# Performance work log

Measured on AMD Instinct MI355X. Metric: run time of the kernel, lower is better.

## Reference

```python
import jax, jax.numpy as jnp
import numpy as np
import math

D_IMG = 768
D_TXT = 512
EPS = 1e-5  # torch LayerNorm default


def setup_inputs() -> dict:
    key = jax.random.key(0)
    ks = jax.random.split(key, 12)
    B, N = 256, 197
    s = 0.02
    return {
        "img_feat": jax.random.normal(ks[0], (B, N, D_IMG), jnp.float32),
        "text_global": jax.random.normal(ks[1], (B, D_TXT), jnp.float32),
        # PatchGCN.msg_proj: Linear(D,D) -> GELU -> Linear(D,D)
        "w1_msg": jax.random.normal(ks[2], (D_IMG, D_IMG), jnp.float32) * s,
        "b1_msg": jnp.zeros((D_IMG,), jnp.float32),
        "w2_msg": jax.random.normal(ks[3], (D_IMG, D_IMG), jnp.float32) * s,
        "b2_msg": jnp.zeros((D_IMG,), jnp.float32),
        "gamma_gcn": jnp.ones((1,), jnp.float32),
        # TGSA.text_proj: Linear(512,768) -> GELU -> Linear(768,768)
        "w1_txt": jax.random.normal(ks[4], (D_TXT, D_IMG), jnp.float32) * s,
        "b1_txt": jnp.zeros((D_IMG,), jnp.float32),
        "w2_txt": jax.random.normal(ks[5], (D_IMG, D_IMG), jnp.float32) * s,
        "b2_txt": jnp.zeros((D_IMG,), jnp.float32),
        "ln_w": jnp.ones((D_IMG,), jnp.float32),
        "ln_b": jnp.zeros((D_IMG,), jnp.float32),
        "gamma": jnp.ones((1,), jnp.float32),
    }


def _layernorm(x, w, b):
    mu = jnp.mean(x, axis=-1, keepdims=True)
    var = jnp.mean(jnp.square(x - mu), axis=-1, keepdims=True)
    return (x - mu) * jax.lax.rsqrt(var + EPS) * w + b


def reference(img_feat, text_global, w1_msg, b1_msg, w2_msg, b2_msg, gamma_gcn,
              w1_txt, b1_txt, w2_txt, b2_txt, ln_w, ln_b, gamma):
    D = img_feat.shape[-1]
    cls_token = img_feat[:, 0:1, :]           # [B,1,D]
    x = img_feat[:, 1:, :]                    # [B,Ns,D]

    # PatchGCN: dense patch self-attention message passing
    attn = jnp.einsum("bnd,bmd->bnm", x, x) / math.sqrt(D)
    A = jax.nn.softmax(attn, axis=-1)
    msg = jnp.einsum("bnm,bmd->bnd", A, x)
    h = jax.nn.gelu(msg @ w1_msg + b1_msg, approximate=False)
    msg = h @ w2_msg + b2_msg
    x = x + gamma_gcn * msg

    # Text-conditioned sigmoid gating
    tq = jax.nn.gelu(text_global @ w1_txt + b1_txt, approximate=False) @ w2_txt + b2_txt
    tq = _layernorm(tq, ln_w, ln_b)            # [B,D]
    mask = jax.nn.sigmoid(jnp.einsum("bnd,bd->bn", x, tq))[..., None]  # [B,Ns,1]
    refined = x + gamma * (x * mask)

    return jnp.concatenate([cls_token, refined], axis=1)
```

## Files before the change

kernel.cpp:

```cpp
#include <hip/hip_runtime.h>
#include <hip/hip_bf16.h>


#define BATCH 256
#define NTOK  196
#define PN    256
#define DIMG  768
#define DTXT  512
#define MROWS (BATCH*NTOK)
#define LN_EPS 1e-5f

typedef __hip_bfloat16 bf16_t;
typedef __hip_bfloat162 bf2_t;
typedef __bf16 bf16x8 __attribute__((ext_vector_type(8)));
typedef float  f32x4  __attribute__((ext_vector_type(4)));

typedef const __attribute__((address_space(1))) void gvoid_t;
typedef __attribute__((address_space(3))) void lvoid_t;

__device__ __forceinline__ float gelu_f(float x){
    return 0.5f * x * (1.0f + erff(x * 0.70710678118654752440f));
}

__global__ void prep_x(const float* __restrict__ img, const float* __restrict__ tq,
                       bf16_t* __restrict__ xb, bf16_t* __restrict__ xt,
                       float* __restrict__ dimg){
    __shared__ float tile[32][33];
    const int b  = blockIdx.z;
    const int m0 = blockIdx.y * 32;
    const int d0 = blockIdx.x * 32;
    const int tx = threadIdx.x, ty = threadIdx.y;
    const float tqv = tq[(size_t)b*DIMG + d0 + tx];
    #pragma unroll
    for (int i = 0; i < 4; i++){
        const int m = m0 + ty + i*8;
        float v = 0.f;
        if (m < NTOK) v = img[((size_t)b*197 + 1 + m)*DIMG + d0 + tx];
        tile[ty + i*8][tx] = v;
        xb[((size_t)b*PN + m)*DIMG + d0 + tx] = __float2bfloat16(v);
        float p = v * tqv;
        #pragma unroll
        for (int o = 1; o < 32; o <<= 1) p += __shfl_xor(p, o);
        if (tx == 0 && m < NTOK) atomicAdd(&dimg[(size_t)b*NTOK + m], p);
    }
    __syncthreads();
    #pragma unroll
    for (int i = 0; i < 4; i++){
        const int d = d0 + ty + i*8;
        xt[((size_t)b*DIMG + d)*PN + m0 + tx] = __float2bfloat16(tile[tx][ty + i*8]);
    }
}

__global__ void prep_w(const float* __restrict__ w, bf16_t* __restrict__ wt){
    __shared__ float tile[32][33];
    const int r0 = blockIdx.y * 32, c0 = blockIdx.x * 32;
    const int tx = threadIdx.x, ty = threadIdx.y;
    #pragma unroll
    for (int i = 0; i < 4; i++)
        tile[ty + i*8][tx] = w[(size_t)(r0 + ty + i*8)*DIMG + c0 + tx];
    __syncthreads();
    #pragma unroll
    for (int i = 0; i < 4; i++)
        wt[(size_t)(c0 + ty + i*8)*DIMG + r0 + tx] = __float2bfloat16(tile[tx][ty + i*8]);
}

__global__ void cls_copy(const float* __restrict__ img, float* __restrict__ out){
    const int i = blockIdx.x * 256 + threadIdx.x;
    const int b = i / DIMG, d = i - b*DIMG;
    out[((size_t)b*197)*DIMG + d] = img[((size_t)b*197)*DIMG + d];
}

__global__ void txt_fc1(const float* __restrict__ text, const float* __restrict__ w,
                        const float* __restrict__ bias, float* __restrict__ h){
    __shared__ float ts[DTXT];
    const int b = blockIdx.y;
    const int n = blockIdx.x * 256 + threadIdx.x;
    for (int k = threadIdx.x; k < DTXT; k += 256) ts[k] = text[(size_t)b*DTXT + k];
    __syncthreads();
    float acc = 0.f;
    for (int k = 0; k < DTXT; k++) acc = fmaf(ts[k], w[(size_t)k*DIMG + n], acc);
    h[(size_t)b*DIMG + n] = gelu_f(acc + bias[n]);
}

__global__ void txt_fc2(const float* __restrict__ h, const float* __restrict__ w,
                        const float* __restrict__ bias, float* __restrict__ tq){
    __shared__ float ts[DIMG];
    const int b = blockIdx.y;
    const int n = blockIdx.x * 256 + threadIdx.x;
    for (int k = threadIdx.x; k < DIMG; k += 256) ts[k] = h[(size_t)b*DIMG + k];
    __syncthreads();
    float acc = 0.f;
    for (int k = 0; k < DIMG; k++) acc = fmaf(ts[k], w[(size_t)k*DIMG + n], acc);
    tq[(size_t)b*DIMG + n] = acc + bias[n];
}

__global__ void txt_ln(float* __restrict__ tq, const float* __restrict__ lw,
                       const float* __restrict__ lb){
    __shared__ float red[4];
    const int b = blockIdx.x, t = threadIdx.x;
    const int wv = t >> 6, lane = t & 63;
    float x[3];
    #pragma unroll
    for (int i = 0; i < 3; i++) x[i] = tq[(size_t)b*DIMG + t + i*256];
    float s = x[0] + x[1] + x[2];
    #pragma unroll
    for (int o = 1; o < 64; o <<= 1) s += __shfl_xor(s, o);
    if (lane == 0) red[wv] = s;
    __syncthreads();
    const float mu = (red[0]+red[1]+red[2]+red[3]) * (1.f/768.f);
    float q = 0.f;
    #pragma unroll
    for (int i = 0; i < 3; i++){ const float d = x[i]-mu; q = fmaf(d, d, q); }
    #pragma unroll
    for (int o = 1; o < 64; o <<= 1) q += __shfl_xor(q, o);
    __syncthreads();
    if (lane == 0) red[wv] = q;
    __syncthreads();
    const float var = (red[0]+red[1]+red[2]+red[3]) * (1.f/768.f);
    const float inv = rsqrtf(var + LN_EPS);
    #pragma unroll
    for (int i = 0; i < 3; i++){
        const int d = t + i*256;
        tq[(size_t)b*DIMG + d] = (x[i]-mu)*inv*lw[d] + lb[d];
    }
}

__global__ void calc_u(const float* __restrict__ tq, const bf16_t* __restrict__ w2T,
                       float* __restrict__ u){
    __shared__ float ts[DIMG];
    const int b = blockIdx.y;
    const int n = blockIdx.x * 256 + threadIdx.x;
    for (int k = threadIdx.x; k < DIMG; k += 256) ts[k] = tq[(size_t)b*DIMG + k];
    __syncthreads();
    float acc = 0.f;
    for (int k = 0; k < DIMG; k++)
        acc = fmaf(ts[k], __bfloat162float(w2T[(size_t)k*DIMG + n]), acc);
    u[(size_t)b*DIMG + n] = acc;
}

__global__ void softmax_k(const float* __restrict__ S, bf16_t* __restrict__ A){
    const int gr = blockIdx.x * 4 + (threadIdx.x >> 6);
    const int lane = threadIdx.x & 63;
    if (gr >= MROWS) return;
    const int b = gr / NTOK, m = gr - b*NTOK;
    const float* row = S + ((size_t)b*PN + m)*PN;
    const float scale = 0.03608439182435161256f;
    float v[4]; float mx = -1e30f;
    #pragma unroll
    for (int i = 0; i < 4; i++){
        const int n = lane + i*64;
        const float val = (n < NTOK) ? row[n]*scale : -1e30f;
        v[i] = val; mx = fmaxf(mx, val);
    }
    #pragma unroll
    for (int o = 1; o < 64; o <<= 1) mx = fmaxf(mx, __shfl_xor(mx, o));
    float sum = 0.f;
    #pragma unroll
    for (int i = 0; i < 4; i++){ v[i] = expf(v[i] - mx); sum += v[i]; }
    #pragma unroll
    for (int o = 1; o < 64; o <<= 1) sum += __shfl_xor(sum, o);
    const float inv = 1.f / sum;
    bf16_t* orow = A + ((size_t)b*PN + m)*PN;
    #pragma unroll
    for (int i = 0; i < 4; i++) orow[lane + i*64] = __float2bfloat16(v[i]*inv);
}

__global__ void scale_k(const bf16_t* __restrict__ h, const float* __restrict__ u,
                        const float* __restrict__ dimg, const float* __restrict__ b2,
                        const float* __restrict__ tq, const float* __restrict__ ggcn,
                        const float* __restrict__ gam, float* __restrict__ scale){
    const int gr = blockIdx.x * 4 + (threadIdx.x >> 6);
    const int lane = threadIdx.x & 63;
    if (gr >= MROWS) return;
    const int b = gr / NTOK;
    const bf16_t* hr = h + (size_t)gr*DIMG;
    const float* ub = u + (size_t)b*DIMG;
    const float* tb = tq + (size_t)b*DIMG;
    float s = 0.f;
    #pragma unroll
    for (int i = 0; i < 6; i++){
        const int d = i*128 + lane*2;
        const bf2_t hv = *(const bf2_t*)(hr + d);
        const float2 uv = *(const float2*)(ub + d);
        const float2 bv = *(const float2*)(b2 + d);
        const float2 tv = *(const float2*)(tb + d);
        s = fmaf(__bfloat162float(hv.x), uv.x, s);
        s = fmaf(__bfloat162float(hv.y), uv.y, s);
        s = fmaf(bv.x, tv.x, s);
        s = fmaf(bv.y, tv.y, s);
    }
    #pragma unroll
    for (int o = 1; o < 64; o <<= 1) s += __shfl_xor(s, o);
    const float dot = dimg[gr] + ggcn[0]*s;
    if (lane == 0)
        scale[gr] = 1.f + gam[0] / (1.f + expf(-dot));
}

template<int MODE>
__global__ __launch_bounds__(256) void gemm_bt(
    const bf16_t* __restrict__ Aall, const bf16_t* __restrict__ Btall,
    int lda, int ldb, int K,
    long long strideA, long long strideB,
    float* __restrict__ outF, bf16_t* __restrict__ outB,
    const float* __restrict__ bias, const float* __restrict__ res,
    const float* __restrict__ gscal, const float* __restrict__ scale)
{
    __shared__ __align__(16) union {
        struct { bf16_t a[128*32]; bf16_t b[128*32]; } s;
        float ep[32*132];
    } sm;
    const int b  = blockIdx.z;
    const int m0 = blockIdx.y * 128;
    const int n0 = blockIdx.x * 128;
    const bf16_t* Ab = Aall + (long long)b * strideA;
    const bf16_t* Bb = Btall + (long long)b * strideB;

    const int t    = threadIdx.x;
    const int lane = t & 63;
    const int wave = t >> 6;
    const int wm   = (wave & 1) * 64;
    const int wn   = (wave >> 1) * 64;
    const int fr   = lane & 15;
    const int quad = lane >> 4;

    f32x4 acc[4][4];
    #pragma unroll
    for (int i = 0; i < 4; i++)
        #pragma unroll
        for (int j = 0; j < 4; j++)
            acc[i][j] = (f32x4){0.f, 0.f, 0.f, 0.f};

    const int lin0 = t, lin1 = t + 256;
    const int r0 = lin0 >> 2, s0 = (lin0 & 3) * 8;
    const int r1 = lin1 >> 2, s1 = (lin1 & 3) * 8;

    for (int k0 = 0; k0 < K; k0 += 32){
        __syncthreads();
        __builtin_amdgcn_global_load_lds((gvoid_t*)(Ab + (long long)(m0+r0)*lda + k0 + s0),
                                         (lvoid_t*)(sm.s.a + lin0*8), 16, 0, 0);
        __builtin_amdgcn_global_load_lds((gvoid_t*)(Ab + (long long)(m0+r1)*lda + k0 + s1),
                                         (lvoid_t*)(sm.s.a + lin1*8), 16, 0, 0);
        __builtin_amdgcn_global_load_lds((gvoid_t*)(Bb + (long long)(n0+r0)*ldb + k0 + s0),
                                         (lvoid_t*)(sm.s.b + lin0*8), 16, 0, 0);
        __builtin_amdgcn_global_load_lds((gvoid_t*)(Bb + (long long)(n0+r1)*ldb + k0 + s1),
                                         (lvoid_t*)(sm.s.b + lin1*8), 16, 0, 0);
        __syncthreads();
        bf16x8 fa[4], fb[4];
        #pragma unroll
        for (int i = 0; i < 4; i++){
            fa[i] = *(const bf16x8*)(sm.s.a + (wm + i*16 + fr)*32 + quad*8);
            fb[i] = *(const bf16x8*)(sm.s.b + (wn + i*16 + fr)*32 + quad*8);
        }
        #pragma unroll
        for (int i = 0; i < 4; i++)
            #pragma unroll
            for (int j = 0; j < 4; j++)
                acc[i][j] = __builtin_amdgcn_mfma_f32_16x16x32_bf16(fa[i], fb[j], acc[i][j], 0, 0, 0);
    }

    const float g = (MODE == 3) ? gscal[0] : 0.f;
    const int lr = t >> 3;
    const int cs = (t & 7) * 16;
    #pragma unroll
    for (int c = 0; c < 4; c++){
        __syncthreads();
        if ((wm == 0) == (c < 2)){
            const int ib = (c & 1) * 2;
            #pragma unroll
            for (int ii = 0; ii < 2; ii++)
                #pragma unroll
                for (int j = 0; j < 4; j++)
                    #pragma unroll
                    for (int r = 0; r < 4; r++)
                        sm.ep[(ii*16 + quad*4 + r)*132 + wn + j*16 + fr] = acc[ib+ii][j][r];
        }
        __syncthreads();
        const int grow = m0 + c*32 + lr;
        float4 v[4];
        const float4* vp = (const float4*)(sm.ep + lr*132 + cs);
        #pragma unroll
        for (int k = 0; k < 4; k++) v[k] = vp[k];

        if (MODE == 0){
            float4* dp = (float4*)(outF + ((long long)b*PN + grow)*PN + n0 + cs);
            #pragma unroll
            for (int k = 0; k < 4; k++) dp[k] = v[k];
        } else if (MODE == 1){
            if (grow < NTOK){
                bf16_t tmp[16];
                #pragma unroll
                for (int k = 0; k < 4; k++){
                    tmp[4*k+0] = __float2bfloat16(v[k].x);
                    tmp[4*k+1] = __float2bfloat16(v[k].y);
                    tmp[4*k+2] = __float2bfloat16(v[k].z);
                    tmp[4*k+3] = __float2bfloat16(v[k].w);
                }
                float4* dp = (float4*)(outB + ((long long)b*NTOK + grow)*DIMG + n0 + cs);
                dp[0] = ((float4*)tmp)[0];
                dp[1] = ((float4*)tmp)[1];
            }
        } else if (MODE == 2){
            const float4* bp = (const float4*)(bias + n0 + cs);
            bf16_t tmp[16];
            #pragma unroll
            for (int k = 0; k < 4; k++){
                const float4 bv = bp[k];
                tmp[4*k+0] = __float2bfloat16(gelu_f(v[k].x + bv.x));
                tmp[4*k+1] = __float2bfloat16(gelu_f(v[k].y + bv.y));
                tmp[4*k+2] = __float2bfloat16(gelu_f(v[k].z + bv.z));
                tmp[4*k+3] = __float2bfloat16(gelu_f(v[k].w + bv.w));
            }
            float4* dp = (float4*)(outB + (long long)grow*DIMG + n0 + cs);
            dp[0] = ((float4*)tmp)[0];
            dp[1] = ((float4*)tmp)[1];
        } else {
            const int bb = grow / NTOK;
            const int nn = grow - bb*NTOK;
            const long long off = ((long long)bb*197 + 1 + nn)*DIMG + n0 + cs;
            const float sc = scale[grow];
            const float4* bp = (const float4*)(bias + n0 + cs);
            const float4* rp = (const float4*)(res + off);
            float4* dp = (float4*)(outF + off);
            #pragma unroll
            for (int k = 0; k < 4; k++){
                const float4 bv = bp[k];
                const float4 rv = rp[k];
                float4 o;
                o.x = (rv.x + g*(v[k].x + bv.x)) * sc;
                o.y = (rv.y + g*(v[k].y + bv.y)) * sc;
                o.z = (rv.z + g*(v[k].z + bv.z)) * sc;
                o.w = (rv.w + g*(v[k].w + bv.w)) * sc;
                dp[k] = o;
            }
        }
    }
}

extern "C" void kernel_launch(void* const* d_in, const int* in_sizes, int n_in,
                              void* d_out, int out_size, void* d_ws, size_t ws_size,
                              hipStream_t stream){
    (void)in_sizes; (void)n_in; (void)out_size;
    const float* img  = (const float*)d_in[0];
    const float* text = (const float*)d_in[1];
    const float* w1m  = (const float*)d_in[2];
    const float* b1m  = (const float*)d_in[3];
    const float* w2m  = (const float*)d_in[4];
    const float* b2m  = (const float*)d_in[5];
    const float* ggcn = (const float*)d_in[6];
    const float* w1t  = (const float*)d_in[7];
    const float* b1t  = (const float*)d_in[8];
    const float* w2t  = (const float*)d_in[9];
    const float* b2t  = (const float*)d_in[10];
    const float* lnw  = (const float*)d_in[11];
    const float* lnb  = (const float*)d_in[12];
    const float* gam  = (const float*)d_in[13];
    float* out = (float*)d_out;

    char* p = (char*)d_ws;
    auto alloc = [&](size_t n){ void* r = (void*)p; p += (n + 255) & ~(size_t)255; return r; };
    bf16_t* x_bf   = (bf16_t*)alloc((size_t)BATCH*PN*DIMG*2);
    bf16_t* xT_bf  = (bf16_t*)alloc((size_t)BATCH*DIMG*PN*2);
    float*  S      = (float*) alloc((size_t)BATCH*PN*PN*4);
    bf16_t* A_bf   = (bf16_t*)alloc((size_t)BATCH*PN*PN*2);
    bf16_t* msg_bf = (bf16_t*)alloc((size_t)MROWS*DIMG*2);
    bf16_t* h_bf   = (bf16_t*)alloc((size_t)MROWS*DIMG*2);
    bf16_t* w1T    = (bf16_t*)alloc((size_t)DIMG*DIMG*2);
    bf16_t* w2T    = (bf16_t*)alloc((size_t)DIMG*DIMG*2);
    float*  htxt   = (float*) alloc((size_t)BATCH*DIMG*4);
    float*  tq     = (float*) alloc((size_t)BATCH*DIMG*4);
    float*  u      = (float*) alloc((size_t)BATCH*DIMG*4);
    float*  dimg   = (float*) alloc((size_t)MROWS*4);
    float*  scl    = (float*) alloc((size_t)MROWS*4);
    if ((size_t)(p - (char*)d_ws) > ws_size) return;

    hipMemsetAsync(dimg, 0, (size_t)MROWS*4, stream);

    txt_fc1<<<dim3(3, BATCH), dim3(256), 0, stream>>>(text, w1t, b1t, htxt);
    txt_fc2<<<dim3(3, BATCH), dim3(256), 0, stream>>>(htxt, w2t, b2t, tq);
    txt_ln<<<dim3(BATCH), dim3(256), 0, stream>>>(tq, lnw, lnb);

    prep_w<<<dim3(24, 24), dim3(32, 8), 0, stream>>>(w1m, w1T);
    prep_w<<<dim3(24, 24), dim3(32, 8), 0, stream>>>(w2m, w2T);
    calc_u<<<dim3(3, BATCH), dim3(256), 0, stream>>>(tq, w2T, u);
    prep_x<<<dim3(24, 8, BATCH), dim3(32, 8), 0, stream>>>(img, tq, x_bf, xT_bf, dimg);
    cls_copy<<<dim3(768), dim3(256), 0, stream>>>(img, out);

    gemm_bt<0><<<dim3(2, 2, BATCH), dim3(256), 0, stream>>>(
        x_bf, x_bf, DIMG, DIMG, DIMG,
        (long long)PN*DIMG, (long long)PN*DIMG, S, nullptr, nullptr, nullptr, nullptr, nullptr);
    softmax_k<<<dim3(MROWS/4), dim3(256), 0, stream>>>(S, A_bf);
    gemm_bt<1><<<dim3(6, 2, BATCH), dim3(256), 0, stream>>>(
        A_bf, xT_bf, PN, PN, PN,
        (long long)PN*PN, (long long)DIMG*PN, nullptr, msg_bf, nullptr, nullptr, nullptr, nullptr);
    gemm_bt<2><<<dim3(6, 392, 1), dim3(256), 0, stream>>>(
        msg_bf, w1T, DIMG, DIMG, DIMG,
        0, 0, nullptr, h_bf, b1m, nullptr, nullptr, nullptr);
    scale_k<<<dim3(MROWS/4), dim3(256), 0, stream>>>(h_bf, u, dimg, b2m, tq, ggcn, gam, scl);
    gemm_bt<3><<<dim3(6, 392, 1), dim3(256), 0, stream>>>(
        h_bf, w2T, DIMG, DIMG, DIMG,
        0, 0, out, nullptr, b2m, img, ggcn, scl);
}
```

Baseline: 928.6 us.

## Fuse patch attention QK^T, softmax and PV into one flash-style kernel

Replaces the separate score GEMM, softmax kernel and A·X GEMM with a single kernel per (batch, 128-row block). It computes scores with MFMA, does the row softmax in registers with cross-wave LDS reductions, stores probabilities in LDS, and multiplies by transposed x tiles. This removes the fp32 S and bf16 A round trips to global memory. It also splits x preparation into a row kernel that computes the text dot directly, with no atomics or memset, plus a bf16 transpose kernel. In exchange the full 256 key rows are recomputed per query block, and only 2 blocks per batch run with heavy register use.

```diff
diff --git a/kernel.cpp b/kernel.cpp
--- a/kernel.cpp
+++ b/kernel.cpp
@@ -9,6 +9,8 @@
 #define DTXT  512
 #define MROWS (BATCH*NTOK)
 #define LN_EPS 1e-5f
+#define LDP   232
+#define FK    224
 
 typedef __hip_bfloat16 bf16_t;
 typedef __hip_bfloat162 bf2_t;
@@ -22,46 +24,60 @@
     return 0.5f * x * (1.0f + erff(x * 0.70710678118654752440f));
 }
 
-__global__ void prep_x(const float* __restrict__ img, const float* __restrict__ tq,
-                       bf16_t* __restrict__ xb, bf16_t* __restrict__ xt,
-                       float* __restrict__ dimg){
-    __shared__ float tile[32][33];
+__global__ void prep_row(const float* __restrict__ img, const float* __restrict__ tq,
+                         bf16_t* __restrict__ xb, float* __restrict__ dimg){
+    const int gr = blockIdx.x * 4 + (threadIdx.x >> 6);
+    const int lane = threadIdx.x & 63;
+    const int b = gr >> 8, m = gr & 255;
+    bf16_t* xrow = xb + ((size_t)b*PN + m)*DIMG;
+    if (m < NTOK){
+        const float* irow = img + ((size_t)b*197 + 1 + m)*DIMG;
+        const float* trow = tq + (size_t)b*DIMG;
+        float dot = 0.f;
+        #pragma unroll
+        for (int i = 0; i < 3; i++){
+            const float4 v = *(const float4*)(irow + lane*4 + i*256);
+            const float4 tv = *(const float4*)(trow + lane*4 + i*256);
+            dot = fmaf(v.x, tv.x, dot); dot = fmaf(v.y, tv.y, dot);
+            dot = fmaf(v.z, tv.z, dot); dot = fmaf(v.w, tv.w, dot);
+            union { bf16_t h[4]; uint2 u; } tmp;
+            tmp.h[0] = __float2bfloat16(v.x); tmp.h[1] = __float2bfloat16(v.y);
+            tmp.h[2] = __float2bfloat16(v.z); tmp.h[3] = __float2bfloat16(v.w);
+            *(uint2*)(xrow + lane*4 + i*256) = tmp.u;
+        }
+        #pragma unroll
+        for (int o = 1; o < 64; o <<= 1) dot += __shfl_xor(dot, o);
+        if (lane == 0) dimg[(size_t)b*NTOK + m] = dot;
+    } else {
+        const uint2 z = {0u, 0u};
+        #pragma unroll
+        for (int i = 0; i < 3; i++)
+            *(uint2*)(xrow + lane*4 + i*256) = z;
+    }
+}
+
+__global__ void prep_xt(const bf16_t* __restrict__ xb, bf16_t* __restrict__ xt){
+    __shared__ unsigned short tile[64*66];
     const int b  = blockIdx.z;
-    const int m0 = blockIdx.y * 32;
-    const int d0 = blockIdx.x * 32;
+    const int m0 = blockIdx.y * 64;
+    const int d0 = blockIdx.x * 64;
     const int tx = threadIdx.x, ty = threadIdx.y;
-    const float tqv = tq[(size_t)b*DIMG + d0 + tx];
-    #pragma unroll
-    for (int i = 0; i < 4; i++){
-        const int m = m0 + ty + i*8;
-        float v = 0.f;
-        if (m < NTOK) v = img[((size_t)b*197 + 1 + m)*DIMG + d0 + tx];
-        tile[ty + i*8][tx] = v;
-        xb[((size_t)b*PN + m)*DIMG + d0 + tx] = __float2bfloat16(v);
-        float p = v * tqv;
-        #pragma unroll
-        for (int o = 1; o < 32; o <<= 1) p += __shfl_xor(p, o);
-        if (tx == 0 && m < NTOK) atomicAdd(&dimg[(size_t)b*NTOK + m], p);
-    }
-    __syncthreads();
-    #pragma unroll
-    for (int i = 0; i < 4; i++){
-        const int d = d0 + ty + i*8;
-        xt[((size_t)b*DIMG + d)*PN + m0 + tx] = __float2bfloat16(tile[tx][ty + i*8]);
-    }
-}
-
-__global__ void prep_w(const float* __restrict__ w, bf16_t* __restrict__ wt){
-    __shared__ float tile[32][33];
-    const int r0 = blockIdx.y * 32, c0 = blockIdx.x * 32;
-    const int tx = threadIdx.x, ty = threadIdx.y;
-    #pragma unroll
-    for (int i = 0; i < 4; i++)
-        tile[ty + i*8][tx] = w[(size_t)(r0 + ty + i*8)*DIMG + c0 + tx];
-    __syncthreads();
-    #pragma unroll
-    for (int i = 0; i < 4; i++)
-        wt[(size_t)(c0 + ty + i*8)*DIMG + r0 + tx] = __float2bfloat16(tile[tx][ty + i*8]);
+    const unsigned short* src = (const unsigned short*)xb;
+    unsigned short* dst = (unsigned short*)xt;
+    #pragma unroll
+    for (int i = 0; i < 8; i++){
+        const int ml = ty + i*8;
+        const unsigned v = *(const unsigned*)(src + ((size_t)b*PN + m0 + ml)*DIMG + d0 + tx*2);
+        *(unsigned*)(tile + ml*66 + tx*2) = v;
+    }
+    __syncthreads();
+    #pragma unroll
+    for (int i = 0; i < 8; i++){
+        const int dl = ty + i*8;
+        const unsigned a = tile[(tx*2    )*66 + dl];
+        const unsigned c = tile[(tx*2 + 1)*66 + dl];
+        *(unsigned*)(dst + ((size_t)b*DIMG + d0 + dl)*PN + m0 + tx*2) = a | (c << 16);
+    }
 }
 
 __global__ void cls_copy(const float* __restrict__ img, float* __restrict__ out){
@@ -125,6 +141,19 @@
     }
 }
 
+__global__ void prep_w(const float* __restrict__ w, bf16_t* __restrict__ wt){
+    __shared__ float tile[32][33];
+    const int r0 = blockIdx.y * 32, c0 = blockIdx.x * 32;
+    const int tx = threadIdx.x, ty = threadIdx.y;
+    #pragma unroll
+    for (int i = 0; i < 4; i++)
+        tile[ty + i*8][tx] = w[(size_t)(r0 + ty + i*8)*DIMG + c0 + tx];
+    __syncthreads();
+    #pragma unroll
+    for (int i = 0; i < 4; i++)
+        wt[(size_t)(c0 + ty + i*8)*DIMG + r0 + tx] = __float2bfloat16(tile[tx][ty + i*8]);
+}
+
 __global__ void calc_u(const float* __restrict__ tq, const bf16_t* __restrict__ w2T,
                        float* __restrict__ u){
     __shared__ float ts[DIMG];
@@ -136,33 +165,6 @@
     for (int k = 0; k < DIMG; k++)
         acc = fmaf(ts[k], __bfloat162float(w2T[(size_t)k*DIMG + n]), acc);
     u[(size_t)b*DIMG + n] = acc;
-}
-
-__global__ void softmax_k(const float* __restrict__ S, bf16_t* __restrict__ A){
-    const int gr = blockIdx.x * 4 + (threadIdx.x >> 6);
-    const int lane = threadIdx.x & 63;
-    if (gr >= MROWS) return;
-    const int b = gr / NTOK, m = gr - b*NTOK;
-    const float* row = S + ((size_t)b*PN + m)*PN;
-    const float scale = 0.03608439182435161256f;
-    float v[4]; float mx = -1e30f;
-    #pragma unroll
-    for (int i = 0; i < 4; i++){
-        const int n = lane + i*64;
-        const float val = (n < NTOK) ? row[n]*scale : -1e30f;
-        v[i] = val; mx = fmaxf(mx, val);
-    }
-    #pragma unroll
-    for (int o = 1; o < 64; o <<= 1) mx = fmaxf(mx, __shfl_xor(mx, o));
-    float sum = 0.f;
-    #pragma unroll
-    for (int i = 0; i < 4; i++){ v[i] = expf(v[i] - mx); sum += v[i]; }
-    #pragma unroll
-    for (int o = 1; o < 64; o <<= 1) sum += __shfl_xor(sum, o);
-    const float inv = 1.f / sum;
-    bf16_t* orow = A + ((size_t)b*PN + m)*PN;
-    #pragma unroll
-    for (int i = 0; i < 4; i++) orow[lane + i*64] = __float2bfloat16(v[i]*inv);
 }
 
 __global__ void scale_k(const bf16_t* __restrict__ h, const float* __restrict__ u,
@@ -196,11 +198,182 @@
         scale[gr] = 1.f + gam[0] / (1.f + expf(-dot));
 }
 
+__global__ __launch_bounds__(256, 2) void flash_attn(
+    const bf16_t* __restrict__ xb, const bf16_t* __restrict__ xt,
+    bf16_t* __restrict__ msg)
+{
+    __shared__ __align__(16) bf16_t Pl[128*LDP];
+    __shared__ __align__(16) bf16_t stage[64*136];
+    __shared__ float redm[2*128];
+    __shared__ float reds[2*128];
+
+    const int b  = blockIdx.y;
+    const int m0 = blockIdx.x * 128;
+    const int t    = threadIdx.x;
+    const int lane = t & 63;
+    const int wave = t >> 6;
+    const int fr   = lane & 15;
+    const int quad = lane >> 4;
+
+    const int wm = (wave & 1) * 64;
+    const int wn = (wave >> 1) * 128;
+    f32x4 acc[4][8];
+    #pragma unroll
+    for (int i = 0; i < 4; i++)
+        #pragma unroll
+        for (int j = 0; j < 8; j++)
+            acc[i][j] = (f32x4){0.f,0.f,0.f,0.f};
+
+    for (int k0 = 0; k0 < DIMG; k0 += 32){
+        __syncthreads();
+        #pragma unroll
+        for (int s = 0; s < 4; s++){
+            const int idx = t + s*256;
+            const int row = idx >> 2, off = (idx & 3) * 8;
+            __builtin_amdgcn_global_load_lds(
+                (gvoid_t*)(xb + ((size_t)b*PN + row)*DIMG + k0 + off),
+                (lvoid_t*)(stage + idx*8), 16, 0, 0);
+        }
+        __syncthreads();
+        #pragma unroll
+        for (int jh = 0; jh < 2; jh++){
+            bf16x8 fa[4], fb[4];
+            #pragma unroll
+            for (int i = 0; i < 4; i++){
+                fa[i] = *(const bf16x8*)(stage + (m0 + wm + i*16 + fr)*32 + quad*8);
+                fb[i] = *(const bf16x8*)(stage + (wn + (jh*4 + i)*16 + fr)*32 + quad*8);
+            }
+            #pragma unroll
+            for (int i = 0; i < 4; i++)
+                #pragma unroll
+                for (int j = 0; j < 4; j++)
+                    acc[i][jh*4 + j] = __builtin_amdgcn_mfma_f32_16x16x32_bf16(
+                        fa[i], fb[j], acc[i][jh*4 + j], 0, 0, 0);
+        }
+    }
+
+    const float sscale = 0.03608439182435161256f;
+    const int wi = wn >> 7;
+    float mx[4][4];
+    #pragma unroll
+    for (int i = 0; i < 4; i++)
+        #pragma unroll
+        for (int r = 0; r < 4; r++){
+            float m_ = -3e38f;
+            #pragma unroll
+            for (int j = 0; j < 8; j++){
+                const bool ok = (wn == 0) || (j*16 + fr < NTOK - 128);
+                if (ok) m_ = fmaxf(m_, acc[i][j][r]*sscale);
+            }
+            #pragma unroll
+            for (int o = 1; o < 16; o <<= 1) m_ = fmaxf(m_, __shfl_xor(m_, o));
+            mx[i][r] = m_;
+            if (fr == 0) redm[wi*128 + wm + i*16 + quad*4 + r] = m_;
+        }
+    __syncthreads();
+    float sm[4][4];
+    #pragma unroll
+    for (int i = 0; i < 4; i++)
+        #pragma unroll
+        for (int r = 0; r < 4; r++){
+            const int row = wm + i*16 + quad*4 + r;
+            const float mxf = fmaxf(redm[row], redm[128 + row]);
+            float s_ = 0.f;
+            #pragma unroll
+            for (int j = 0; j < 8; j++){
+                const bool ok = (wn == 0) || (j*16 + fr < NTOK - 128);
+                const float p = ok ? __expf(acc[i][j][r]*sscale - mxf) : 0.f;
+                acc[i][j][r] = p;
+                s_ += p;
+            }
+            #pragma unroll
+            for (int o = 1; o < 16; o <<= 1) s_ += __shfl_xor(s_, o);
+            if (fr == 0) reds[wi*128 + row] = s_;
+        }
+    __syncthreads();
+    #pragma unroll
+    for (int i = 0; i < 4; i++)
+        #pragma unroll
+        for (int r = 0; r < 4; r++){
+            const int row = wm + i*16 + quad*4 + r;
+            const float inv = 1.f / (reds[row] + reds[128 + row]);
+            #pragma unroll
+            for (int j = 0; j < 8; j++){
+                const int col = wn + j*16 + fr;
+                if (col < LDP)
+                    Pl[row*LDP + col] = __float2bfloat16(acc[i][j][r] * inv);
+            }
+        }
+    __syncthreads();
+
+    const int wm2 = (wave & 1) * 64;
+    const int wn2 = (wave >> 1) * 64;
+    for (int nt = 0; nt < 6; nt++){
+        const int n0 = nt * 128;
+        f32x4 acc2[4][4];
+        #pragma unroll
+        for (int i = 0; i < 4; i++)
+            #pragma unroll
+            for (int j = 0; j < 4; j++)
+                acc2[i][j] = (f32x4){0.f,0.f,0.f,0.f};
+
+        for (int k0 = 0; k0 < FK; k0 += 32){
+            __syncthreads();
+            #pragma unroll
+            for (int s = 0; s < 2; s++){
+                const int idx = t + s*256;
+                const int row = idx >> 2, off = (idx & 3) * 8;
+                __builtin_amdgcn_global_load_lds(
+                    (gvoid_t*)(xt + ((size_t)b*DIMG + n0 + row)*PN + k0 + off),
+                    (lvoid_t*)(stage + idx*8), 16, 0, 0);
+            }
+            __syncthreads();
+            bf16x8 fa[4], fb[4];
+            #pragma unroll
+            for (int i = 0; i < 4; i++){
+                fa[i] = *(const bf16x8*)(Pl + (wm2 + i*16 + fr)*LDP + k0 + quad*8);
+                fb[i] = *(const bf16x8*)(stage + (wn2 + i*16 + fr)*32 + quad*8);
+            }
+            #pragma unroll
+            for (int i = 0; i < 4; i++)
+                #pragma unroll
+                for (int j = 0; j < 4; j++)
+                    acc2[i][j] = __builtin_amdgcn_mfma_f32_16x16x32_bf16(
+                        fa[i], fb[j], acc2[i][j], 0, 0, 0);
+        }
+
+        #pragma unroll
+        for (int c = 0; c < 2; c++){
+            __syncthreads();
+            if (wm2 == c*64){
+                #pragma unroll
+                for (int i = 0; i < 4; i++)
+                    #pragma unroll
+                    for (int j = 0; j < 4; j++)
+                        #pragma unroll
+                        for (int r = 0; r < 4; r++)
+                            stage[(i*16 + quad*4 + r)*136 + wn2 + j*16 + fr] =
+                                __float2bfloat16(acc2[i][j][r]);
+            }
+            __syncthreads();
+            const int lr = t >> 2;
+            const int grow = m0 + c*64 + lr;
+            if (grow < NTOK){
+                const int col0 = (t & 3) * 32;
+                bf16_t* dst = msg + ((size_t)b*NTOK + grow)*DIMG + n0 + col0;
+                const bf16_t* srcp = stage + lr*136 + col0;
+                #pragma unroll
+                for (int u2 = 0; u2 < 4; u2++)
+                    *(uint4*)(dst + u2*8) = *(const uint4*)(srcp + u2*8);
+            }
+        }
+    }
+}
+
 template<int MODE>
 __global__ __launch_bounds__(256) void gemm_bt(
     const bf16_t* __restrict__ Aall, const bf16_t* __restrict__ Btall,
     int lda, int ldb, int K,
-    long long strideA, long long strideB,
     float* __restrict__ outF, bf16_t* __restrict__ outB,
     const float* __restrict__ bias, const float* __restrict__ res,
     const float* __restrict__ gscal, const float* __restrict__ scale)
@@ -209,11 +382,8 @@
         struct { bf16_t a[128*32]; bf16_t b[128*32]; } s;
         float ep[32*132];
     } sm;
-    const int b  = blockIdx.z;
     const int m0 = blockIdx.y * 128;
     const int n0 = blockIdx.x * 128;
-    const bf16_t* Ab = Aall + (long long)b * strideA;
-    const bf16_t* Bb = Btall + (long long)b * strideB;
 
     const int t    = threadIdx.x;
     const int lane = t & 63;
@@ -236,13 +406,13 @@
 
     for (int k0 = 0; k0 < K; k0 += 32){
         __syncthreads();
-        __builtin_amdgcn_global_load_lds((gvoid_t*)(Ab + (long long)(m0+r0)*lda + k0 + s0),
+        __builtin_amdgcn_global_load_lds((gvoid_t*)(Aall + (size_t)(m0+r0)*lda + k0 + s0),
                                          (lvoid_t*)(sm.s.a + lin0*8), 16, 0, 0);
-        __builtin_amdgcn_global_load_lds((gvoid_t*)(Ab + (long long)(m0+r1)*lda + k0 + s1),
+        __builtin_amdgcn_global_load_lds((gvoid_t*)(Aall + (size_t)(m0+r1)*lda + k0 + s1),
                                          (lvoid_t*)(sm.s.a + lin1*8), 16, 0, 0);
-        __builtin_amdgcn_global_load_lds((gvoid_t*)(Bb + (long long)(n0+r0)*ldb + k0 + s0),
+        __builtin_amdgcn_global_load_lds((gvoid_t*)(Btall + (size_t)(n0+r0)*ldb + k0 + s0),
                                          (lvoid_t*)(sm.s.b + lin0*8), 16, 0, 0);
-        __builtin_amdgcn_global_load_lds((gvoid_t*)(Bb + (long long)(n0+r1)*ldb + k0 + s1),
+        __builtin_amdgcn_global_load_lds((gvoid_t*)(Btall + (size_t)(n0+r1)*ldb + k0 + s1),
                                          (lvoid_t*)(sm.s.b + lin1*8), 16, 0, 0);
         __syncthreads();
         bf16x8 fa[4], fb[4];
@@ -281,25 +451,7 @@
         #pragma unroll
         for (int k = 0; k < 4; k++) v[k] = vp[k];
 
-        if (MODE == 0){
-            float4* dp = (float4*)(outF + ((long long)b*PN + grow)*PN + n0 + cs);
-            #pragma unroll
-            for (int k = 0; k < 4; k++) dp[k] = v[k];
-        } else if (MODE == 1){
-            if (grow < NTOK){
-                bf16_t tmp[16];
-                #pragma unroll
-                for (int k = 0; k < 4; k++){
-                    tmp[4*k+0] = __float2bfloat16(v[k].x);
-                    tmp[4*k+1] = __float2bfloat16(v[k].y);
-                    tmp[4*k+2] = __float2bfloat16(v[k].z);
-                    tmp[4*k+3] = __float2bfloat16(v[k].w);
-                }
-                float4* dp = (float4*)(outB + ((long long)b*NTOK + grow)*DIMG + n0 + cs);
-                dp[0] = ((float4*)tmp)[0];
-                dp[1] = ((float4*)tmp)[1];
-            }
-        } else if (MODE == 2){
+        if (MODE == 2){
             const float4* bp = (const float4*)(bias + n0 + cs);
             bf16_t tmp[16];
             #pragma unroll
@@ -310,13 +462,13 @@
                 tmp[4*k+2] = __float2bfloat16(gelu_f(v[k].z + bv.z));
                 tmp[4*k+3] = __float2bfloat16(gelu_f(v[k].w + bv.w));
             }
-            float4* dp = (float4*)(outB + (long long)grow*DIMG + n0 + cs);
+            float4* dp = (float4*)(outB + (size_t)grow*DIMG + n0 + cs);
             dp[0] = ((float4*)tmp)[0];
             dp[1] = ((float4*)tmp)[1];
         } else {
             const int bb = grow / NTOK;
             const int nn = grow - bb*NTOK;
-            const long long off = ((long long)bb*197 + 1 + nn)*DIMG + n0 + cs;
+            const size_t off = ((size_t)bb*197 + 1 + nn)*DIMG + n0 + cs;
             const float sc = scale[grow];
             const float4* bp = (const float4*)(bias + n0 + cs);
             const float4* rp = (const float4*)(res + off);
@@ -360,8 +512,6 @@
     auto alloc = [&](size_t n){ void* r = (void*)p; p += (n + 255) & ~(size_t)255; return r; };
     bf16_t* x_bf   = (bf16_t*)alloc((size_t)BATCH*PN*DIMG*2);
     bf16_t* xT_bf  = (bf16_t*)alloc((size_t)BATCH*DIMG*PN*2);
-    float*  S      = (float*) alloc((size_t)BATCH*PN*PN*4);
-    bf16_t* A_bf   = (bf16_t*)alloc((size_t)BATCH*PN*PN*2);
     bf16_t* msg_bf = (bf16_t*)alloc((size_t)MROWS*DIMG*2);
     bf16_t* h_bf   = (bf16_t*)alloc((size_t)MROWS*DIMG*2);
     bf16_t* w1T    = (bf16_t*)alloc((size_t)DIMG*DIMG*2);
@@ -373,8 +523,6 @@
     float*  scl    = (float*) alloc((size_t)MROWS*4);
     if ((size_t)(p - (char*)d_ws) > ws_size) return;
 
-    hipMemsetAsync(dimg, 0, (size_t)MROWS*4, stream);
-
     txt_fc1<<<dim3(3, BATCH), dim3(256), 0, stream>>>(text, w1t, b1t, htxt);
     txt_fc2<<<dim3(3, BATCH), dim3(256), 0, stream>>>(htxt, w2t, b2t, tq);
     txt_ln<<<dim3(BATCH), dim3(256), 0, stream>>>(tq, lnw, lnb);
@@ -382,21 +530,15 @@
     prep_w<<<dim3(24, 24), dim3(32, 8), 0, stream>>>(w1m, w1T);
     prep_w<<<dim3(24, 24), dim3(32, 8), 0, stream>>>(w2m, w2T);
     calc_u<<<dim3(3, BATCH), dim3(256), 0, stream>>>(tq, w2T, u);
-    prep_x<<<dim3(24, 8, BATCH), dim3(32, 8), 0, stream>>>(img, tq, x_bf, xT_bf, dimg);
+    prep_row<<<dim3(BATCH*PN/4), dim3(256), 0, stream>>>(img, tq, x_bf, dimg);
+    prep_xt<<<dim3(12, 4, BATCH), dim3(32, 8), 0, stream>>>(x_bf, xT_bf);
     cls_copy<<<dim3(768), dim3(256), 0, stream>>>(img, out);
 
-    gemm_bt<0><<<dim3(2, 2, BATCH), dim3(256), 0, stream>>>(
-        x_bf, x_bf, DIMG, DIMG, DIMG,
-        (long long)PN*DIMG, (long long)PN*DIMG, S, nullptr, nullptr, nullptr, nullptr, nullptr);
-    softmax_k<<<dim3(MROWS/4), dim3(256), 0, stream>>>(S, A_bf);
-    gemm_bt<1><<<dim3(6, 2, BATCH), dim3(256), 0, stream>>>(
-        A_bf, xT_bf, PN, PN, PN,
-        (long long)PN*PN, (long long)DIMG*PN, nullptr, msg_bf, nullptr, nullptr, nullptr, nullptr);
-    gemm_bt<2><<<dim3(6, 392, 1), dim3(256), 0, stream>>>(
-        msg_bf, w1T, DIMG, DIMG, DIMG,
-        0, 0, nullptr, h_bf, b1m, nullptr, nullptr, nullptr);
+    flash_attn<<<dim3(2, BATCH), dim3(256), 0, stream>>>(x_bf, xT_bf, msg_bf);
+
+    gemm_bt<2><<<dim3(6, 392), dim3(256), 0, stream>>>(
+        msg_bf, w1T, DIMG, DIMG, DIMG, nullptr, h_bf, b1m, nullptr, nullptr, nullptr);
     scale_k<<<dim3(MROWS/4), dim3(256), 0, stream>>>(h_bf, u, dimg, b2m, tq, ggcn, gam, scl);
-    gemm_bt<3><<<dim3(6, 392, 1), dim3(256), 0, stream>>>(
-        h_bf, w2T, DIMG, DIMG, DIMG,
-        0, 0, out, nullptr, b2m, img, ggcn, scl);
-}
+    gemm_bt<3><<<dim3(6, 392), dim3(256), 0, stream>>>(
+        h_bf, w2T, DIMG, DIMG, DIMG, out, nullptr, b2m, img, ggcn, scl);
+}
```

Result: faster. 809.2 us (-12.9%).
